# Performance work log

Hardware: AMD Instinct MI355X
Metric: run time of the kernel (lower is better)

## Reference

```python
import jax, jax.numpy as jnp
import numpy as np

D_MODEL, D_STATE, D_CONV, EXPAND = 2048, 16, 4, 2
D_INNER = EXPAND * D_MODEL            # 4096
DT_RANK = -(-D_MODEL // 16)           # 128
B_SZ, L = 2, 1024


def setup_inputs() -> dict:
    key = jax.random.key(0)
    ks = jax.random.split(key, 10)
    s = 0.02
    return {
        "hidden_states": jax.random.normal(ks[0], (B_SZ, L, D_MODEL), jnp.float32),
        "in_proj_w": jax.random.normal(ks[1], (2 * D_INNER, D_MODEL), jnp.float32) * s,
        "conv_w": jax.random.normal(ks[2], (D_INNER, D_CONV), jnp.float32) * 0.1,
        "conv_b": jax.random.normal(ks[3], (D_INNER,), jnp.float32) * 0.1,
        "x_proj_w": jax.random.normal(ks[4], (DT_RANK + 2 * D_STATE, D_INNER), jnp.float32) * s,
        "dt_proj_w": jax.random.normal(ks[5], (D_INNER, DT_RANK), jnp.float32) * s,
        "dt_proj_b": jax.random.normal(ks[6], (D_INNER,), jnp.float32) * 0.1 - 4.0,
        "A": -jax.random.uniform(ks[7], (D_INNER, D_STATE), jnp.float32, 1.0, 16.0),
        "D": jnp.ones((D_INNER,), jnp.float32),
        "out_proj_w": jax.random.normal(ks[8], (D_MODEL, D_INNER), jnp.float32) * s,
    }


def _mamba_forward(hidden_states, in_proj_w, conv_w, conv_b, x_proj_w,
                   dt_proj_w, dt_proj_b, A, D, out_proj_w):
    # in_proj: [B,L,d_model] -> [B,L,2*d_inner]; chunk into x and gate
    proj = jnp.einsum('bld,ed->ble', hidden_states, in_proj_w)
    x, gate = jnp.split(proj, 2, axis=-1)            # each [B,L,d_inner]

    # depthwise causal conv1d over time + SiLU
    xc = x.transpose(0, 2, 1)                        # [B,d_inner,L]
    xc = jax.lax.conv_general_dilated(
        xc, conv_w[:, None, :],                      # kernel [d_inner,1,d_conv]
        window_strides=(1,), padding=[(D_CONV - 1, 0)],
        feature_group_count=D_INNER,
        dimension_numbers=('NCH', 'OIH', 'NCH'))
    xc = jax.nn.silu(xc + conv_b[None, :, None])
    xt = xc.transpose(0, 2, 1)                       # [B,L,d_inner]

    # x_proj -> (dt_rank, d_state, d_state)
    ssm = jnp.einsum('bld,ed->ble', xt, x_proj_w)
    ts, Bm, Cm = jnp.split(ssm, [DT_RANK, DT_RANK + D_STATE], axis=-1)
    dt = jnp.einsum('blr,dr->bld', ts, dt_proj_w)    # dt_proj (skip_bias_add)
    dt = jax.nn.softplus(dt + dt_proj_b)             # delta_softplus with bias

    # selective scan over time
    def step(state, inp):
        dt_t, x_t, B_t, C_t = inp                    # [B,di],[B,di],[B,ds],[B,ds]
        dA = jnp.exp(dt_t[..., None] * A)            # [B,d_inner,d_state]
        dBx = dt_t[..., None] * B_t[:, None, :] * x_t[..., None]
        state = state * dA + dBx
        y = jnp.einsum('bds,bs->bd', state, C_t)
        return state, y

    xs = (dt.transpose(1, 0, 2), xt.transpose(1, 0, 2),
          Bm.transpose(1, 0, 2), Cm.transpose(1, 0, 2))
    state0 = jnp.zeros((hidden_states.shape[0], D_INNER, D_STATE), jnp.float32)
    _, ys = jax.lax.scan(step, state0, xs)           # [L,B,d_inner]
    y = ys.transpose(1, 0, 2) + xt * D               # D skip connection
    y = y * jax.nn.silu(gate)                        # gating (z in selective scan)

    return jnp.einsum('bld,ed->ble', y, out_proj_w)  # out_proj -> [B,L,d_model]


def reference(hidden_states, in_proj_w, conv_w, conv_b, x_proj_w,
              dt_proj_w, dt_proj_b, A, D, out_proj_w):
    return _mamba_forward(hidden_states, in_proj_w, conv_w, conv_b, x_proj_w,
                          dt_proj_w, dt_proj_b, A, D, out_proj_w)
```

## Files before the change

kernel.cpp:

```cpp
#include <hip/hip_runtime.h>
#include <hip/hip_bf16.h>
#include <math.h>

#define B_SZ    2
#define LSEQ    1024
#define D_MODEL 2048
#define D_INNER 4096
#define D_STATE 16
#define DT_RANK 128
#define M_TOK   (B_SZ * LSEQ)
#define NCHUNK  16
#define LCHUNK  (LSEQ / NCHUNK)

typedef __attribute__((ext_vector_type(8))) short bf16x8;
typedef __attribute__((ext_vector_type(4))) float f32x4;

__device__ __forceinline__ float softplusf_(float x) {
    return fmaxf(x, 0.f) + log1pf(expf(-fabsf(x)));
}
__device__ __forceinline__ unsigned f2bf(float f) {
    union { float f; unsigned u; } v; v.f = f;
    const unsigned u = v.u;
    return (u + 0x7fffu + ((u >> 16) & 1u)) >> 16;
}
__device__ __forceinline__ float bf2f(unsigned u) {
    union { unsigned u; float f; } v; v.u = u << 16; return v.f;
}
__device__ __forceinline__ void gload16(const void* g, void* lds) {
    __builtin_amdgcn_global_load_lds(
        (const __attribute__((address_space(1))) void*)g,
        (__attribute__((address_space(3))) void*)lds, 16, 0, 0);
}

__global__ __launch_bounds__(256, 2)
void gemm_bf16_bt(const ushort* __restrict__ A, int lda,
                  const ushort* __restrict__ B, int ldb,
                  void* __restrict__ Cv, int ldc,
                  void* __restrict__ Cv2,
                  const float* __restrict__ bias,
                  int M, int N, int K, int epi, size_t zstride)
{
    __shared__ ushort As[2][128 * 64];
    __shared__ ushort Bs[2][128 * 64];
    const int t    = threadIdx.x;
    const int bm   = blockIdx.y << 7, bn = blockIdx.x << 7;
    const int wave = t >> 6, lane = t & 63;
    const int wr   = (wave >> 1) << 6, wc = (wave & 1) << 6;
    const int lr   = lane & 15, lh = lane >> 4;
    const int kper  = K / gridDim.z;
    const int kbase = blockIdx.z * kper;
    const int nkt   = kper >> 6;

    const ushort* ga[4]; const ushort* gb[4];
    int ci[4];
#pragma unroll
    for (int it = 0; it < 4; ++it) {
        const int flat = t + (it << 8);
        const int row  = flat >> 3, j = flat & 7;
        const int jj   = j ^ (row & 7);
        ga[it] = A + (size_t)(bm + row) * lda + kbase + jj * 8;
        int gn = bn + row; gn = gn < N ? gn : N - 1;
        gb[it] = B + (size_t)gn * ldb + kbase + jj * 8;
        ci[it] = (it << 2) + wave;
    }

#define STAGE(bsel) do {                                                \
    _Pragma("unroll")                                                   \
    for (int it = 0; it < 4; ++it) {                                    \
        gload16(ga[it], &As[bsel][ci[it] * 512]);                       \
        gload16(gb[it], &Bs[bsel][ci[it] * 512]);                       \
        ga[it] += 64; gb[it] += 64;                                     \
    }                                                                   \
} while (0)

    f32x4 acc[4][4];
#pragma unroll
    for (int i = 0; i < 4; ++i)
#pragma unroll
        for (int j = 0; j < 4; ++j) {
            acc[i][j][0] = 0.f; acc[i][j][1] = 0.f;
            acc[i][j][2] = 0.f; acc[i][j][3] = 0.f;
        }

    STAGE(0);
    for (int kt = 0; kt < nkt; ++kt) {
        const int cur = kt & 1;
        if (kt + 1 < nkt) {
            STAGE(cur ^ 1);
            asm volatile("s_waitcnt vmcnt(8)" ::: "memory");
        } else {
            asm volatile("s_waitcnt vmcnt(0)" ::: "memory");
        }
        __builtin_amdgcn_s_barrier();
        __builtin_amdgcn_sched_barrier(0);
        const char* Ab = (const char*)As[cur];
        const char* Bb = (const char*)Bs[cur];
#pragma unroll
        for (int kk = 0; kk < 2; ++kk) {
            bf16x8 af[4], bf[4];
#pragma unroll
            for (int mi = 0; mi < 4; ++mi) {
                const int row = wr + (mi << 4) + lr;
                const int ch  = ((kk << 2) + lh) ^ (row & 7);
                af[mi] = *(const bf16x8*)(Ab + row * 128 + (ch << 4));
            }
#pragma unroll
            for (int nj = 0; nj < 4; ++nj) {
                const int row = wc + (nj << 4) + lr;
                const int ch  = ((kk << 2) + lh) ^ (row & 7);
                bf[nj] = *(const bf16x8*)(Bb + row * 128 + (ch << 4));
            }
#pragma unroll
            for (int mi = 0; mi < 4; ++mi)
#pragma unroll
                for (int nj = 0; nj < 4; ++nj)
                    acc[mi][nj] = __builtin_amdgcn_mfma_f32_16x16x32_bf16(
                        af[mi], bf[nj], acc[mi][nj], 0, 0, 0);
        }
        __builtin_amdgcn_s_barrier();
        __builtin_amdgcn_sched_barrier(0);
    }
#undef STAGE

    float*  C  = (float*)Cv + (size_t)blockIdx.z * zstride;
    ushort* Cb = (ushort*)Cv;
    ushort* C2 = (ushort*)Cv2;
#pragma unroll
    for (int mi = 0; mi < 4; ++mi) {
#pragma unroll
        for (int nj = 0; nj < 4; ++nj) {
            const int col  = bn + wc + (nj << 4) + lr;
            const int row0 = bm + wr + (mi << 4) + (lh << 2);
            if (col < N) {
#pragma unroll
                for (int r = 0; r < 4; ++r) {
                    const float v = acc[mi][nj][r];
                    if (epi == 0) {
                        C[(size_t)(row0 + r) * ldc + col] = v;
                    } else if (epi == 1) {
                        Cb[(size_t)(row0 + r) * ldc + col] =
                            (ushort)f2bf(softplusf_(v + bias[col]));
                    } else {
                        if (col < D_INNER)
                            Cb[(size_t)(row0 + r) * ldc + col] = (ushort)f2bf(v);
                        else
                            C2[(size_t)(row0 + r) * ldc + (col - D_INNER)] = (ushort)f2bf(v);
                    }
                }
            }
        }
    }
}

__global__ __launch_bounds__(256)
void cvt_bf16(const float* __restrict__ in, ushort* __restrict__ out, int n8)
{
    for (int i = blockIdx.x * 256 + threadIdx.x; i < n8; i += gridDim.x * 256) {
        const float4 v0 = ((const float4*)in)[i * 2];
        const float4 v1 = ((const float4*)in)[i * 2 + 1];
        int4 p;
        p.x = (int)(f2bf(v0.x) | (f2bf(v0.y) << 16));
        p.y = (int)(f2bf(v0.z) | (f2bf(v0.w) << 16));
        p.z = (int)(f2bf(v1.x) | (f2bf(v1.y) << 16));
        p.w = (int)(f2bf(v1.z) | (f2bf(v1.w) << 16));
        ((int4*)out)[i] = p;
    }
}

__global__ __launch_bounds__(256)
void reduce_out(const float* __restrict__ part, float* __restrict__ out, int n4)
{
    for (int i = blockIdx.x * 256 + threadIdx.x; i < n4; i += gridDim.x * 256) {
        const float4 a = ((const float4*)part)[i];
        const float4 b = ((const float4*)(part + (size_t)M_TOK * D_MODEL))[i];
        ((float4*)out)[i] = make_float4(a.x + b.x, a.y + b.y, a.z + b.z, a.w + b.w);
    }
}

__global__ __launch_bounds__(256)
void conv_silu_k(const ushort* __restrict__ xraw,
                 const float* __restrict__ cw,
                 const float* __restrict__ cb,
                 ushort* __restrict__ xb)
{
    const int d = (blockIdx.x << 8) + threadIdx.x;
    const int m = blockIdx.y;
    const int l = m & (LSEQ - 1);
    const float4 w = *(const float4*)&cw[d << 2];
    const float wv[4] = {w.x, w.y, w.z, w.w};
    float acc = cb[d];
#pragma unroll
    for (int j = 0; j < 4; ++j) {
        const int ls = l - 3 + j;
        if (ls >= 0)
            acc = fmaf(wv[j], bf2f(xraw[(size_t)(m - 3 + j) * D_INNER + d]), acc);
    }
    const float sg = 1.f / (1.f + expf(-acc));
    xb[(size_t)m * D_INNER + d] = (ushort)f2bf(acc * sg);
}

__global__ __launch_bounds__(256)
void reduce_ssm(const float* __restrict__ part,
                float* __restrict__ ssmf, ushort* __restrict__ ssmb)
{
    const int i = blockIdx.x * 256 + threadIdx.x;
    float v = 0.f;
#pragma unroll
    for (int z = 0; z < 8; ++z) v += part[(size_t)z * (M_TOK * 160) + i];
    ssmf[i] = v;
    ssmb[i] = (ushort)f2bf(v);
}

__global__ __launch_bounds__(256)
void scan_pass1(const ushort* __restrict__ dtp,
                const ushort* __restrict__ xb,
                const float* __restrict__ ssm,
                const float* __restrict__ Ap,
                float* __restrict__ Pc, float* __restrict__ Qc)
{
    const int d = (blockIdx.x << 8) + threadIdx.x;
    const int c = blockIdx.y, b = blockIdx.z;
    float a[16];
    *(float4*)&a[0]  = *(const float4*)&Ap[d * 16];
    *(float4*)&a[4]  = *(const float4*)&Ap[d * 16 + 4];
    *(float4*)&a[8]  = *(const float4*)&Ap[d * 16 + 8];
    *(float4*)&a[12] = *(const float4*)&Ap[d * 16 + 12];
    float q[16];
#pragma unroll
    for (int s = 0; s < 16; ++s) q[s] = 0.f;
    float dtsum = 0.f;
    const size_t m0 = (size_t)b * LSEQ + (size_t)c * LCHUNK;
#pragma unroll 2
    for (int l = 0; l < LCHUNK; ++l) {
        const size_t m = m0 + l;
        const float dt = bf2f(dtp[m * D_INNER + d]);
        const float xv = bf2f(xb[m * D_INNER + d]);
        const float4 B0 = *(const float4*)&ssm[m * 160 + 128];
        const float4 B1 = *(const float4*)&ssm[m * 160 + 132];
        const float4 B2 = *(const float4*)&ssm[m * 160 + 136];
        const float4 B3 = *(const float4*)&ssm[m * 160 + 140];
        const float Bv[16] = {B0.x,B0.y,B0.z,B0.w, B1.x,B1.y,B1.z,B1.w,
                              B2.x,B2.y,B2.z,B2.w, B3.x,B3.y,B3.z,B3.w};
        const float t1 = dt * xv;
#pragma unroll
        for (int s = 0; s < 16; ++s) {
            const float dA = __expf(dt * a[s]);
            q[s] = fmaf(q[s], dA, t1 * Bv[s]);
        }
        dtsum += dt;
    }
    const size_t o = (((size_t)b * D_INNER + d) * NCHUNK + c) * D_STATE;
    float P[16];
#pragma unroll
    for (int s = 0; s < 16; ++s) P[s] = __expf(a[s] * dtsum);
#pragma unroll
    for (int s4 = 0; s4 < 4; ++s4) {
        *(float4*)&Pc[o + s4 * 4] = make_float4(P[s4*4], P[s4*4+1], P[s4*4+2], P[s4*4+3]);
        *(float4*)&Qc[o + s4 * 4] = make_float4(q[s4*4], q[s4*4+1], q[s4*4+2], q[s4*4+3]);
    }
}

__global__ __launch_bounds__(256)
void scan_pass2(const float* __restrict__ Pc, float* __restrict__ Qc)
{
    const int i = blockIdx.x * 256 + threadIdx.x;
    const size_t base = (size_t)(i >> 4) * (NCHUNK * D_STATE) + (i & 15);
    float st = 0.f;
#pragma unroll
    for (int c = 0; c < NCHUNK; ++c) {
        const float P = Pc[base + c * D_STATE];
        const float q = Qc[base + c * D_STATE];
        Qc[base + c * D_STATE] = st;
        st = fmaf(st, P, q);
    }
}

__global__ __launch_bounds__(256)
void scan_pass3(const ushort* __restrict__ dtp,
                ushort* __restrict__ xb,
                const ushort* __restrict__ gb,
                const float* __restrict__ ssm,
                const float* __restrict__ Ap,
                const float* __restrict__ Qc,
                const float* __restrict__ Dp)
{
    const int d = (blockIdx.x << 8) + threadIdx.x;
    const int c = blockIdx.y, b = blockIdx.z;
    float a[16], st[16];
    *(float4*)&a[0]  = *(const float4*)&Ap[d * 16];
    *(float4*)&a[4]  = *(const float4*)&Ap[d * 16 + 4];
    *(float4*)&a[8]  = *(const float4*)&Ap[d * 16 + 8];
    *(float4*)&a[12] = *(const float4*)&Ap[d * 16 + 12];
    const size_t qo = (((size_t)b * D_INNER + d) * NCHUNK + c) * D_STATE;
    *(float4*)&st[0]  = *(const float4*)&Qc[qo];
    *(float4*)&st[4]  = *(const float4*)&Qc[qo + 4];
    *(float4*)&st[8]  = *(const float4*)&Qc[qo + 8];
    *(float4*)&st[12] = *(const float4*)&Qc[qo + 12];
    const float Dd = Dp[d];
    const size_t m0 = (size_t)b * LSEQ + (size_t)c * LCHUNK;
#pragma unroll 2
    for (int l = 0; l < LCHUNK; ++l) {
        const size_t m = m0 + l;
        const float dt = bf2f(dtp[m * D_INNER + d]);
        const float xv = bf2f(xb[m * D_INNER + d]);
        const float gv = bf2f(gb[m * D_INNER + d]);
        const float4 B0 = *(const float4*)&ssm[m * 160 + 128];
        const float4 B1 = *(const float4*)&ssm[m * 160 + 132];
        const float4 B2 = *(const float4*)&ssm[m * 160 + 136];
        const float4 B3 = *(const float4*)&ssm[m * 160 + 140];
        const float4 C0 = *(const float4*)&ssm[m * 160 + 144];
        const float4 C1 = *(const float4*)&ssm[m * 160 + 148];
        const float4 C2 = *(const float4*)&ssm[m * 160 + 152];
        const float4 C3 = *(const float4*)&ssm[m * 160 + 156];
        const float Bv[16] = {B0.x,B0.y,B0.z,B0.w, B1.x,B1.y,B1.z,B1.w,
                              B2.x,B2.y,B2.z,B2.w, B3.x,B3.y,B3.z,B3.w};
        const float Cv[16] = {C0.x,C0.y,C0.z,C0.w, C1.x,C1.y,C1.z,C1.w,
                              C2.x,C2.y,C2.z,C2.w, C3.x,C3.y,C3.z,C3.w};
        const float t1 = dt * xv;
        float y = 0.f;
#pragma unroll
        for (int s = 0; s < 16; ++s) {
            const float dA = __expf(dt * a[s]);
            st[s] = fmaf(st[s], dA, t1 * Bv[s]);
            y = fmaf(st[s], Cv[s], y);
        }
        const float yg  = fmaf(Dd, xv, y);
        const float sig = 1.f / (1.f + expf(-gv));
        xb[m * D_INNER + d] = (ushort)f2bf(yg * (gv * sig));
    }
}

extern "C" void kernel_launch(void* const* d_in, const int* in_sizes, int n_in,
                              void* d_out, int out_size, void* d_ws, size_t ws_size,
                              hipStream_t stream)
{
    (void)in_sizes; (void)n_in; (void)out_size; (void)ws_size;
    const float* hs  = (const float*)d_in[0];
    const float* inw = (const float*)d_in[1];
    const float* cw  = (const float*)d_in[2];
    const float* cb  = (const float*)d_in[3];
    const float* xw  = (const float*)d_in[4];
    const float* dtw = (const float*)d_in[5];
    const float* dtb = (const float*)d_in[6];
    const float* Ap  = (const float*)d_in[7];
    const float* Dp  = (const float*)d_in[8];
    const float* ow  = (const float*)d_in[9];
    float* out = (float*)d_out;

    float*  ws    = (float*)d_ws;
    ushort* pg    = (ushort*)(ws + 0);
    ushort* xraw  = (ushort*)(ws + 4194304);
    ushort* xtb   = (ushort*)(ws + 8388608);
    float*  ssmf  = ws + 12582912;
    ushort* ssmb  = (ushort*)(ws + 12910592);
    ushort* xwb   = (ushort*)(ws + 13074432);
    ushort* dtwb  = (ushort*)(ws + 13402112);
    ushort* hsb   = (ushort*)(ws + 13664256);
    ushort* inwb  = (ushort*)(ws + 15761408);
    ushort* owb   = (ushort*)(ws + 15761408);
    float*  part  = ws + 19955712;
    ushort* dtb16 = (ushort*)(ws + 19955712);
    float*  Pc    = ws + 4194304;
    float*  Qc    = ws + 6291456;
    float*  opart = ws + 0;

    const dim3 blk(256);

    cvt_bf16<<<dim3(1280), blk, 0, stream>>>(hs,  hsb,  524288);
    cvt_bf16<<<dim3(1280), blk, 0, stream>>>(inw, inwb, 2097152);
    cvt_bf16<<<dim3(1280), blk, 0, stream>>>(xw,  xwb,  81920);
    cvt_bf16<<<dim3(1280), blk, 0, stream>>>(dtw, dtwb, 65536);

    gemm_bf16_bt<<<dim3(64, 16, 1), blk, 0, stream>>>(
        hsb, D_MODEL, inwb, D_MODEL, xraw, D_INNER, pg, nullptr,
        M_TOK, 2 * D_INNER, D_MODEL, 5, 0);

    cvt_bf16<<<dim3(1280), blk, 0, stream>>>(ow, owb, 1048576);

    conv_silu_k<<<dim3(16, M_TOK), blk, 0, stream>>>(xraw, cw, cb, xtb);

    gemm_bf16_bt<<<dim3(2, 16, 8), blk, 0, stream>>>(
        xtb, D_INNER, xwb, D_INNER, part, 160, nullptr, nullptr,
        M_TOK, 160, D_INNER, 0, (size_t)M_TOK * 160);
    reduce_ssm<<<dim3(1280), blk, 0, stream>>>(part, ssmf, ssmb);

    gemm_bf16_bt<<<dim3(32, 16, 1), blk, 0, stream>>>(
        ssmb, 160, dtwb, DT_RANK, dtb16, D_INNER, nullptr, dtb,
        M_TOK, D_INNER, DT_RANK, 1, 0);

    scan_pass1<<<dim3(16, NCHUNK, B_SZ), blk, 0, stream>>>(dtb16, xtb, ssmf, Ap, Pc, Qc);
    scan_pass2<<<dim3((B_SZ * D_INNER * D_STATE) / 256), blk, 0, stream>>>(Pc, Qc);
    scan_pass3<<<dim3(16, NCHUNK, B_SZ), blk, 0, stream>>>(dtb16, xtb, pg, ssmf, Ap, Qc, Dp);

    gemm_bf16_bt<<<dim3(16, 16, 2), blk, 0, stream>>>(
        xtb, D_INNER, owb, D_INNER, opart, D_MODEL, nullptr, nullptr,
        M_TOK, D_MODEL, D_INNER, 0, (size_t)M_TOK * D_MODEL);
    reduce_out<<<dim3(1024), blk, 0, stream>>>(opart, out, (M_TOK * D_MODEL) / 4);
}
```

Baseline: 351.7 us.

## Use three-stage LDS pipeline with BK=32, block swizzle, and higher occupancy in GEMM

Restructures the bf16 GEMM from a double-buffered BK=64 pipeline to a triple-buffered BK=32 pipeline with a new XOR swizzle for the narrower rows. It also remaps workgroup IDs so that neighbouring groups are spread in strides of eight, and raises launch bounds to 3 blocks per CU. LDS use per block stays the same while prefetch depth increases, and higher occupancy is meant to hide global-load latency. The cost is twice as many barriers per unit of K and possible register pressure from the tighter launch bound.

```diff
diff --git a/kernel.cpp b/kernel.cpp
--- a/kernel.cpp
+++ b/kernel.cpp
@@ -32,7 +32,7 @@
         (__attribute__((address_space(3))) void*)lds, 16, 0, 0);
 }
 
-__global__ __launch_bounds__(256, 2)
+__global__ __launch_bounds__(256, 3)
 void gemm_bf16_bt(const ushort* __restrict__ A, int lda,
                   const ushort* __restrict__ B, int ldb,
                   void* __restrict__ Cv, int ldc,
@@ -40,36 +40,43 @@
                   const float* __restrict__ bias,
                   int M, int N, int K, int epi, size_t zstride)
 {
-    __shared__ ushort As[2][128 * 64];
-    __shared__ ushort Bs[2][128 * 64];
-    const int t    = threadIdx.x;
-    const int bm   = blockIdx.y << 7, bn = blockIdx.x << 7;
+    __shared__ ushort As[3][128 * 32];
+    __shared__ ushort Bs[3][128 * 32];
+    const int t = threadIdx.x;
+
+    const int nwg = gridDim.x * gridDim.y;
+    int wg = blockIdx.x + gridDim.x * blockIdx.y;
+    wg = (wg & 7) * (nwg >> 3) + (wg >> 3);
+    const int bx = wg % gridDim.x, by = wg / gridDim.x;
+    const int bm = by << 7, bn = bx << 7;
+
     const int wave = t >> 6, lane = t & 63;
     const int wr   = (wave >> 1) << 6, wc = (wave & 1) << 6;
     const int lr   = lane & 15, lh = lane >> 4;
     const int kper  = K / gridDim.z;
     const int kbase = blockIdx.z * kper;
-    const int nkt   = kper >> 6;
-
-    const ushort* ga[4]; const ushort* gb[4];
-    int ci[4];
-#pragma unroll
-    for (int it = 0; it < 4; ++it) {
-        const int flat = t + (it << 8);
-        const int row  = flat >> 3, j = flat & 7;
-        const int jj   = j ^ (row & 7);
+    const int nkt   = kper >> 5;
+
+    const ushort* ga[2]; const ushort* gb[2];
+    int ldof[2];
+#pragma unroll
+    for (int it = 0; it < 2; ++it) {
+        const int seg = (it << 2) + wave;
+        const int c   = (seg << 6) + lane;
+        const int row = c >> 2, j = c & 3;
+        const int jj  = j ^ ((row >> 1) & 3);
         ga[it] = A + (size_t)(bm + row) * lda + kbase + jj * 8;
         int gn = bn + row; gn = gn < N ? gn : N - 1;
         gb[it] = B + (size_t)gn * ldb + kbase + jj * 8;
-        ci[it] = (it << 2) + wave;
-    }
-
-#define STAGE(bsel) do {                                                \
+        ldof[it] = seg << 9;
+    }
+
+#define STAGE(bi) do {                                                  \
     _Pragma("unroll")                                                   \
-    for (int it = 0; it < 4; ++it) {                                    \
-        gload16(ga[it], &As[bsel][ci[it] * 512]);                       \
-        gload16(gb[it], &Bs[bsel][ci[it] * 512]);                       \
-        ga[it] += 64; gb[it] += 64;                                     \
+    for (int it = 0; it < 2; ++it) {                                    \
+        gload16(ga[it], &As[bi][ldof[it]]);                             \
+        gload16(gb[it], &Bs[bi][ldof[it]]);                             \
+        ga[it] += 32; gb[it] += 32;                                     \
     }                                                                   \
 } while (0)
 
@@ -83,40 +90,45 @@
         }
 
     STAGE(0);
+    STAGE(1);
+    int cur = 0, stg = 2;
     for (int kt = 0; kt < nkt; ++kt) {
-        const int cur = kt & 1;
-        if (kt + 1 < nkt) {
-            STAGE(cur ^ 1);
+        const int rem = nkt - 1 - kt;
+        if (rem >= 2) {
+            STAGE(stg);
+            stg = (stg == 2) ? 0 : stg + 1;
             asm volatile("s_waitcnt vmcnt(8)" ::: "memory");
+        } else if (rem == 1) {
+            asm volatile("s_waitcnt vmcnt(4)" ::: "memory");
         } else {
             asm volatile("s_waitcnt vmcnt(0)" ::: "memory");
         }
         __builtin_amdgcn_s_barrier();
         __builtin_amdgcn_sched_barrier(0);
+
         const char* Ab = (const char*)As[cur];
         const char* Bb = (const char*)Bs[cur];
-#pragma unroll
-        for (int kk = 0; kk < 2; ++kk) {
-            bf16x8 af[4], bf[4];
-#pragma unroll
-            for (int mi = 0; mi < 4; ++mi) {
-                const int row = wr + (mi << 4) + lr;
-                const int ch  = ((kk << 2) + lh) ^ (row & 7);
-                af[mi] = *(const bf16x8*)(Ab + row * 128 + (ch << 4));
-            }
-#pragma unroll
-            for (int nj = 0; nj < 4; ++nj) {
-                const int row = wc + (nj << 4) + lr;
-                const int ch  = ((kk << 2) + lh) ^ (row & 7);
-                bf[nj] = *(const bf16x8*)(Bb + row * 128 + (ch << 4));
-            }
-#pragma unroll
-            for (int mi = 0; mi < 4; ++mi)
-#pragma unroll
-                for (int nj = 0; nj < 4; ++nj)
-                    acc[mi][nj] = __builtin_amdgcn_mfma_f32_16x16x32_bf16(
-                        af[mi], bf[nj], acc[mi][nj], 0, 0, 0);
-        }
+        bf16x8 af[4], bf[4];
+#pragma unroll
+        for (int mi = 0; mi < 4; ++mi) {
+            const int row = wr + (mi << 4) + lr;
+            const int ch  = lh ^ ((row >> 1) & 3);
+            af[mi] = *(const bf16x8*)(Ab + row * 64 + (ch << 4));
+        }
+#pragma unroll
+        for (int nj = 0; nj < 4; ++nj) {
+            const int row = wc + (nj << 4) + lr;
+            const int ch  = lh ^ ((row >> 1) & 3);
+            bf[nj] = *(const bf16x8*)(Bb + row * 64 + (ch << 4));
+        }
+#pragma unroll
+        for (int mi = 0; mi < 4; ++mi)
+#pragma unroll
+            for (int nj = 0; nj < 4; ++nj)
+                acc[mi][nj] = __builtin_amdgcn_mfma_f32_16x16x32_bf16(
+                    af[mi], bf[nj], acc[mi][nj], 0, 0, 0);
+
+        cur = (cur == 2) ? 0 : cur + 1;
         __builtin_amdgcn_s_barrier();
         __builtin_amdgcn_sched_barrier(0);
     }
```

After: 393.3 us. +11.8%, slower.

## Use 8-wave GEMM blocks and sliding-window conv over 64-token runs

Applied to the files above, without the earlier changes.

The GEMM now runs 512 threads (8 waves) per 128x128 tile, each wave computing a 64x32 sub-tile, so per-wave accumulators and loads are halved and more waves are available to hide latency. The load mapping and vmcnt wait count are adjusted to match. The conv+SiLU kernel now has each thread walk 64 consecutive tokens, keeping the last three inputs in registers instead of reloading four values per output. This trades fewer blocks and more serial work per thread in the conv for reduced redundant loads, and adds more B-fragment LDS reads per MFMA in the GEMM.

```diff
diff --git a/kernel.cpp b/kernel.cpp
--- a/kernel.cpp
+++ b/kernel.cpp
@@ -32,7 +32,7 @@
         (__attribute__((address_space(3))) void*)lds, 16, 0, 0);
 }
 
-__global__ __launch_bounds__(256, 2)
+__global__ __launch_bounds__(512, 4)
 void gemm_bf16_bt(const ushort* __restrict__ A, int lda,
                   const ushort* __restrict__ B, int ldb,
                   void* __restrict__ Cv, int ldc,
@@ -45,39 +45,40 @@
     const int t    = threadIdx.x;
     const int bm   = blockIdx.y << 7, bn = blockIdx.x << 7;
     const int wave = t >> 6, lane = t & 63;
-    const int wr   = (wave >> 1) << 6, wc = (wave & 1) << 6;
+    const int wr   = (wave >> 2) << 6;
+    const int wc   = (wave & 3) << 5;
     const int lr   = lane & 15, lh = lane >> 4;
     const int kper  = K / gridDim.z;
     const int kbase = blockIdx.z * kper;
     const int nkt   = kper >> 6;
 
-    const ushort* ga[4]; const ushort* gb[4];
-    int ci[4];
-#pragma unroll
-    for (int it = 0; it < 4; ++it) {
-        const int flat = t + (it << 8);
-        const int row  = flat >> 3, j = flat & 7;
-        const int jj   = j ^ (row & 7);
+    const ushort* ga[2]; const ushort* gb[2];
+    int ldof[2];
+#pragma unroll
+    for (int it = 0; it < 2; ++it) {
+        const int seg = wave + (it << 3);
+        const int row = (seg << 3) + (lane >> 3);
+        const int jj  = (lane & 7) ^ ((lane >> 3) & 7);
         ga[it] = A + (size_t)(bm + row) * lda + kbase + jj * 8;
         int gn = bn + row; gn = gn < N ? gn : N - 1;
         gb[it] = B + (size_t)gn * ldb + kbase + jj * 8;
-        ci[it] = (it << 2) + wave;
+        ldof[it] = seg << 9;
     }
 
 #define STAGE(bsel) do {                                                \
     _Pragma("unroll")                                                   \
-    for (int it = 0; it < 4; ++it) {                                    \
-        gload16(ga[it], &As[bsel][ci[it] * 512]);                       \
-        gload16(gb[it], &Bs[bsel][ci[it] * 512]);                       \
+    for (int it = 0; it < 2; ++it) {                                    \
+        gload16(ga[it], &As[bsel][ldof[it]]);                           \
+        gload16(gb[it], &Bs[bsel][ldof[it]]);                           \
         ga[it] += 64; gb[it] += 64;                                     \
     }                                                                   \
 } while (0)
 
-    f32x4 acc[4][4];
+    f32x4 acc[4][2];
 #pragma unroll
     for (int i = 0; i < 4; ++i)
 #pragma unroll
-        for (int j = 0; j < 4; ++j) {
+        for (int j = 0; j < 2; ++j) {
             acc[i][j][0] = 0.f; acc[i][j][1] = 0.f;
             acc[i][j][2] = 0.f; acc[i][j][3] = 0.f;
         }
@@ -87,17 +88,18 @@
         const int cur = kt & 1;
         if (kt + 1 < nkt) {
             STAGE(cur ^ 1);
-            asm volatile("s_waitcnt vmcnt(8)" ::: "memory");
+            asm volatile("s_waitcnt vmcnt(4)" ::: "memory");
         } else {
             asm volatile("s_waitcnt vmcnt(0)" ::: "memory");
         }
         __builtin_amdgcn_s_barrier();
         __builtin_amdgcn_sched_barrier(0);
+
         const char* Ab = (const char*)As[cur];
         const char* Bb = (const char*)Bs[cur];
 #pragma unroll
         for (int kk = 0; kk < 2; ++kk) {
-            bf16x8 af[4], bf[4];
+            bf16x8 af[4], bf[2];
 #pragma unroll
             for (int mi = 0; mi < 4; ++mi) {
                 const int row = wr + (mi << 4) + lr;
@@ -105,7 +107,7 @@
                 af[mi] = *(const bf16x8*)(Ab + row * 128 + (ch << 4));
             }
 #pragma unroll
-            for (int nj = 0; nj < 4; ++nj) {
+            for (int nj = 0; nj < 2; ++nj) {
                 const int row = wc + (nj << 4) + lr;
                 const int ch  = ((kk << 2) + lh) ^ (row & 7);
                 bf[nj] = *(const bf16x8*)(Bb + row * 128 + (ch << 4));
@@ -113,7 +115,7 @@
 #pragma unroll
             for (int mi = 0; mi < 4; ++mi)
 #pragma unroll
-                for (int nj = 0; nj < 4; ++nj)
+                for (int nj = 0; nj < 2; ++nj)
                     acc[mi][nj] = __builtin_amdgcn_mfma_f32_16x16x32_bf16(
                         af[mi], bf[nj], acc[mi][nj], 0, 0, 0);
         }
@@ -128,7 +130,7 @@
 #pragma unroll
     for (int mi = 0; mi < 4; ++mi) {
 #pragma unroll
-        for (int nj = 0; nj < 4; ++nj) {
+        for (int nj = 0; nj < 2; ++nj) {
             const int col  = bn + wc + (nj << 4) + lr;
             const int row0 = bm + wr + (mi << 4) + (lh << 2);
             if (col < N) {
@@ -183,20 +185,30 @@
                  const float* __restrict__ cb,
                  ushort* __restrict__ xb)
 {
-    const int d = (blockIdx.x << 8) + threadIdx.x;
-    const int m = blockIdx.y;
-    const int l = m & (LSEQ - 1);
+    const int d  = (blockIdx.x << 8) + threadIdx.x;
+    const int m0 = blockIdx.y << 6;
+    const int l0 = m0 & (LSEQ - 1);
     const float4 w = *(const float4*)&cw[d << 2];
-    const float wv[4] = {w.x, w.y, w.z, w.w};
-    float acc = cb[d];
-#pragma unroll
-    for (int j = 0; j < 4; ++j) {
-        const int ls = l - 3 + j;
-        if (ls >= 0)
-            acc = fmaf(wv[j], bf2f(xraw[(size_t)(m - 3 + j) * D_INNER + d]), acc);
-    }
-    const float sg = 1.f / (1.f + expf(-acc));
-    xb[(size_t)m * D_INNER + d] = (ushort)f2bf(acc * sg);
+    const float bias = cb[d];
+    float x3 = 0.f, x2 = 0.f, x1 = 0.f;
+    if (l0 > 0) {
+        x3 = bf2f(xraw[(size_t)(m0 - 3) * D_INNER + d]);
+        x2 = bf2f(xraw[(size_t)(m0 - 2) * D_INNER + d]);
+        x1 = bf2f(xraw[(size_t)(m0 - 1) * D_INNER + d]);
+    }
+#pragma unroll 4
+    for (int i = 0; i < 64; ++i) {
+        const size_t m = (size_t)m0 + i;
+        const float x0 = bf2f(xraw[m * D_INNER + d]);
+        float acc = bias;
+        acc = fmaf(w.x, x3, acc);
+        acc = fmaf(w.y, x2, acc);
+        acc = fmaf(w.z, x1, acc);
+        acc = fmaf(w.w, x0, acc);
+        const float sg = 1.f / (1.f + expf(-acc));
+        xb[m * D_INNER + d] = (ushort)f2bf(acc * sg);
+        x3 = x2; x2 = x1; x1 = x0;
+    }
 }
 
 __global__ __launch_bounds__(256)
@@ -365,26 +377,27 @@
     float*  opart = ws + 0;
 
     const dim3 blk(256);
+    const dim3 blk512(512);
 
     cvt_bf16<<<dim3(1280), blk, 0, stream>>>(hs,  hsb,  524288);
     cvt_bf16<<<dim3(1280), blk, 0, stream>>>(inw, inwb, 2097152);
     cvt_bf16<<<dim3(1280), blk, 0, stream>>>(xw,  xwb,  81920);
     cvt_bf16<<<dim3(1280), blk, 0, stream>>>(dtw, dtwb, 65536);
 
-    gemm_bf16_bt<<<dim3(64, 16, 1), blk, 0, stream>>>(
+    gemm_bf16_bt<<<dim3(64, 16, 1), blk512, 0, stream>>>(
         hsb, D_MODEL, inwb, D_MODEL, xraw, D_INNER, pg, nullptr,
         M_TOK, 2 * D_INNER, D_MODEL, 5, 0);
 
     cvt_bf16<<<dim3(1280), blk, 0, stream>>>(ow, owb, 1048576);
 
-    conv_silu_k<<<dim3(16, M_TOK), blk, 0, stream>>>(xraw, cw, cb, xtb);
-
-    gemm_bf16_bt<<<dim3(2, 16, 8), blk, 0, stream>>>(
+    conv_silu_k<<<dim3(16, 32), blk, 0, stream>>>(xraw, cw, cb, xtb);
+
+    gemm_bf16_bt<<<dim3(2, 16, 8), blk512, 0, stream>>>(
         xtb, D_INNER, xwb, D_INNER, part, 160, nullptr, nullptr,
         M_TOK, 160, D_INNER, 0, (size_t)M_TOK * 160);
     reduce_ssm<<<dim3(1280), blk, 0, stream>>>(part, ssmf, ssmb);
 
-    gemm_bf16_bt<<<dim3(32, 16, 1), blk, 0, stream>>>(
+    gemm_bf16_bt<<<dim3(32, 16, 1), blk512, 0, stream>>>(
         ssmb, 160, dtwb, DT_RANK, dtb16, D_INNER, nullptr, dtb,
         M_TOK, D_INNER, DT_RANK, 1, 0);
 
@@ -392,7 +405,7 @@
     scan_pass2<<<dim3((B_SZ * D_INNER * D_STATE) / 256), blk, 0, stream>>>(Pc, Qc);
     scan_pass3<<<dim3(16, NCHUNK, B_SZ), blk, 0, stream>>>(dtb16, xtb, pg, ssmf, Ap, Qc, Dp);
 
-    gemm_bf16_bt<<<dim3(16, 16, 2), blk, 0, stream>>>(
+    gemm_bf16_bt<<<dim3(16, 16, 2), blk512, 0, stream>>>(
         xtb, D_INNER, owb, D_INNER, opart, D_MODEL, nullptr, nullptr,
         M_TOK, D_MODEL, D_INNER, 0, (size_t)M_TOK * D_MODEL);
     reduce_out<<<dim3(1024), blk, 0, stream>>>(opart, out, (M_TOK * D_MODEL) / 4);
```

Result: faster. 324.1 us (-7.9%).
